# Optimization experiments

Hardware: AMD Instinct MI355X
Metric: run time of the kernel (lower is better)

The kernel has to match this reference:

```python
import jax, jax.numpy as jnp
import numpy as np

T, B, F, H = 128, 32768, 8, 64


def gru_step(h, x, Wih, Whh, bih, bhh):
    # PyTorch GRU cell, gate order (r, z, n)
    gi = x @ Wih.T + bih          # [B, 3H]
    gh = h @ Whh.T + bhh          # [B, 3H]
    i_r, i_z, i_n = jnp.split(gi, 3, axis=-1)
    h_r, h_z, h_n = jnp.split(gh, 3, axis=-1)
    r = jax.nn.sigmoid(i_r + h_r)
    z = jax.nn.sigmoid(i_z + h_z)
    n = jnp.tanh(i_n + r * h_n)
    return (1.0 - z) * n + z * h


def setup_inputs() -> dict:
    key = jax.random.key(0)
    ks = jax.random.split(key, 12)
    s = 0.1  # small init scale
    return {
        "inputs": jax.random.normal(ks[0], (T, B, F), jnp.float32),
        "target": jax.random.normal(ks[1], (T, B, F), jnp.float32),
        "enc_Wih": jax.random.normal(ks[2], (3 * H, F), jnp.float32) * s,
        "enc_Whh": jax.random.normal(ks[3], (3 * H, H), jnp.float32) * s,
        "enc_bih": jax.random.normal(ks[4], (3 * H,), jnp.float32) * s,
        "enc_bhh": jax.random.normal(ks[5], (3 * H,), jnp.float32) * s,
        "dec_Wih": jax.random.normal(ks[6], (3 * H, F), jnp.float32) * s,
        "dec_Whh": jax.random.normal(ks[7], (3 * H, H), jnp.float32) * s,
        "dec_bih": jax.random.normal(ks[8], (3 * H,), jnp.float32) * s,
        "dec_bhh": jax.random.normal(ks[9], (3 * H,), jnp.float32) * s,
        "out_W": jax.random.normal(ks[10], (F, H), jnp.float32) * s,
        "out_b": jax.random.normal(ks[11], (F,), jnp.float32) * s,
    }


def reference(inputs, target, enc_Wih, enc_Whh, enc_bih, enc_bhh,
              dec_Wih, dec_Whh, dec_bih, dec_bhh, out_W, out_b):
    batch = inputs.shape[1]
    # ---- Encoder: single-layer GRU over T steps, h0 = 0 ----
    h0 = jnp.zeros((batch, H), inputs.dtype)

    def enc_body(h, x_t):
        h = gru_step(h, x_t, enc_Wih, enc_Whh, enc_bih, enc_bhh)
        return h, None

    enc_hidden, _ = jax.lax.scan(enc_body, h0, inputs)

    # ---- Decoder: teacher forcing; input at t=0 is zeros, then target[t-1] ----
    dec_in = jnp.concatenate(
        [jnp.zeros((1, batch, target.shape[2]), target.dtype), target[:-1]], axis=0)

    def dec_body(h, x_t):
        h = gru_step(h, x_t, dec_Wih, dec_Whh, dec_bih, dec_bhh)
        y = h @ out_W.T + out_b  # [B, F]
        return h, y

    _, decoder_outputs = jax.lax.scan(dec_body, enc_hidden, dec_in)
    return decoder_outputs  # [T, B, F]
```

## Files before the change

### kernel.cpp

```cpp
#include <hip/hip_runtime.h>

#define T_STEPS 128
#define B_SIZE  32768
#define F_DIM   8
#define H_DIM   64

#define BLOCK_THREADS 128
#define GRID_BLOCKS   (B_SIZE / 16)

typedef float f32x4 __attribute__((ext_vector_type(4)));
typedef short bfrag __attribute__((ext_vector_type(8)));
typedef unsigned int u32x4 __attribute__((ext_vector_type(4)));

#define MFMA16(A, B, C) __builtin_amdgcn_mfma_f32_16x16x32_bf16((A), (B), (C), 0, 0, 0)

__device__ __forceinline__ short f2bf(float f) { return __builtin_bit_cast(short, (__bf16)f); }
__device__ __forceinline__ float4 ld4(const void* p) { return *(const float4*)p; }

constexpr float S1 = 1.4426950408889634f;
constexpr float S2 = 2.f * S1;


__global__ __launch_bounds__(BLOCK_THREADS, 3)
void seq2seq_split_kernel(const float* __restrict__ inputs, const float* __restrict__ target,
                          const float* __restrict__ eWih, const float* __restrict__ eWhh,
                          const float* __restrict__ ebih, const float* __restrict__ ebhh,
                          const float* __restrict__ dWih, const float* __restrict__ dWhh,
                          const float* __restrict__ dbih, const float* __restrict__ dbhh,
                          const float* __restrict__ oW, const float* __restrict__ ob,
                          float* __restrict__ out)
{
    __shared__ u32x4 sXT[2][6][64];
    __shared__ u32x4 sEx[2][2][64];

    const int tid  = threadIdx.x;
    const int lane = tid & 63;
    const int w    = tid >> 6;
    const int c    = lane & 15;
    const int g    = lane >> 4;
    const long samp = (long)blockIdx.x * 16 + c;

    bfrag wr[2][2], wz[2][2], whn[2][2];
    f32x4 bhn[2];

    auto load_phase = [&](const float* __restrict__ Wih, const float* __restrict__ Whh,
                          const float* __restrict__ bih, const float* __restrict__ bhh) {
        __syncthreads();
#pragma unroll
        for (int tl = 0; tl < 2; ++tl) {
            const int tt = 2 * w + tl;
            const int rowR = 16 * tt + c, rowZ = rowR + 64, rowN = rowR + 128;
#pragma unroll
            for (int j = 0; j < 2; ++j) {
                const int kt = (j == 0) ? w : 1 - w;
                bfrag fr, fz, fn;
#pragma unroll
                for (int e = 0; e < 8; ++e) {
                    const int k = 32 * kt + 16 * (e >> 2) + 4 * g + (e & 3);
                    fr[e] = f2bf(Whh[rowR * H_DIM + k] * S1);
                    fz[e] = f2bf(Whh[rowZ * H_DIM + k] * S1);
                    fn[e] = f2bf(Whh[rowN * H_DIM + k] * S2);
                }
                wr[tl][j] = fr; wz[tl][j] = fz; whn[tl][j] = fn;
            }
            bfrag xr, xz, xnw;
#pragma unroll
            for (int e = 0; e < 8; ++e) {
                const int k = 16 * (e >> 2) + 4 * g + (e & 3);
                float vr = 0.f, vz = 0.f, vn = 0.f;
                if (k < F_DIM) {
                    vr = Wih[rowR * F_DIM + k]; vz = Wih[rowZ * F_DIM + k]; vn = Wih[rowN * F_DIM + k];
                } else if (k == F_DIM) {
                    vr = bih[rowR] + bhh[rowR]; vz = bih[rowZ] + bhh[rowZ]; vn = bih[rowN];
                }
                xr[e] = f2bf(vr * S1); xz[e] = f2bf(vz * S1); xnw[e] = f2bf(vn * S2);
            }
            sXT[w][3 * tl + 0][lane] = __builtin_bit_cast(u32x4, xr);
            sXT[w][3 * tl + 1][lane] = __builtin_bit_cast(u32x4, xz);
            sXT[w][3 * tl + 2][lane] = __builtin_bit_cast(u32x4, xnw);
#pragma unroll
            for (int r4 = 0; r4 < 4; ++r4) bhn[tl][r4] = bhh[128 + 16 * tt + 4 * g + r4] * S2;
        }
        __syncthreads();
    };

    f32x4 hc[2] = {{0.f, 0.f, 0.f, 0.f}, {0.f, 0.f, 0.f, 0.f}};
    bfrag hl = (bfrag){0, 0, 0, 0, 0, 0, 0, 0};
    bfrag ho = (bfrag){0, 0, 0, 0, 0, 0, 0, 0};
    bfrag bx0 = (bfrag){0, 0, 0, 0, 0, 0, 0, 0};
    if (g == 2) bx0[0] = f2bf(1.f);

    const u32x4* xt = &sXT[w][0][lane];

    auto step = [&](const bfrag bx) {
#pragma unroll
        for (int tl = 0; tl < 2; ++tl) {
            const bfrag xr  = __builtin_bit_cast(bfrag, xt[(3 * tl + 0) * 64]);
            const bfrag xz  = __builtin_bit_cast(bfrag, xt[(3 * tl + 1) * 64]);
            const bfrag xnw = __builtin_bit_cast(bfrag, xt[(3 * tl + 2) * 64]);
            f32x4 aR = {0.f, 0.f, 0.f, 0.f}, aZ = {0.f, 0.f, 0.f, 0.f};
            f32x4 aIN = {0.f, 0.f, 0.f, 0.f};
            f32x4 aHN = bhn[tl];
            aR = MFMA16(wr[tl][0], hl, aR);  aR = MFMA16(wr[tl][1], ho, aR);  aR = MFMA16(xr, bx, aR);
            aZ = MFMA16(wz[tl][0], hl, aZ);  aZ = MFMA16(wz[tl][1], ho, aZ);  aZ = MFMA16(xz, bx, aZ);
            aHN = MFMA16(whn[tl][0], hl, aHN); aHN = MFMA16(whn[tl][1], ho, aHN);
            aIN = MFMA16(xnw, bx, aIN);
#pragma unroll
            for (int r4 = 0; r4 < 4; ++r4) {
                const float rg = __builtin_amdgcn_rcpf(1.f + __builtin_amdgcn_exp2f(-aR[r4]));
                const float zg = __builtin_amdgcn_rcpf(1.f + __builtin_amdgcn_exp2f(-aZ[r4]));
                const float np = aIN[r4] + rg * aHN[r4];
                const float ng = 1.f - 2.f * __builtin_amdgcn_rcpf(__builtin_amdgcn_exp2f(np) + 1.f);
                hc[tl][r4] = ng + zg * (hc[tl][r4] - ng);
            }
        }
        bfrag nl;
#pragma unroll
        for (int e = 0; e < 8; ++e) nl[e] = f2bf(hc[e >> 2][e & 3]);
        hl = nl;
    };

    load_phase(eWih, eWhh, ebih, ebhh);
    int p = 0;
    const unsigned istep = B_SIZE * F_DIM * 4;
    unsigned ioff = (unsigned)((samp * F_DIM + 4 * g) * 4);
    float4 xn = make_float4(0.f, 0.f, 0.f, 0.f);
    if (g < 2) xn = ld4((const char*)inputs + ioff);
    ioff += istep;
#pragma unroll 1
    for (int t = 0; t < T_STEPS; ++t) {
        const float4 xv = xn;
        if (g < 2 && t + 1 < T_STEPS) xn = ld4((const char*)inputs + ioff);
        ioff += istep;
        bfrag bx = bx0;
        if (g < 2) { bx[0] = f2bf(xv.x); bx[1] = f2bf(xv.y); bx[2] = f2bf(xv.z); bx[3] = f2bf(xv.w); }
        step(bx);
        sEx[p][w][lane] = __builtin_bit_cast(u32x4, hl);
        __syncthreads();
        ho = __builtin_bit_cast(bfrag, sEx[p][w ^ 1][lane]);
        p ^= 1;
    }

    load_phase(dWih, dWhh, dbih, dbhh);
    bfrag wo[2];
    f32x4 obv;
#pragma unroll
    for (int j = 0; j < 2; ++j)
#pragma unroll
        for (int e = 0; e < 8; ++e) {
            const int k = 32 * j + 16 * (e >> 2) + 4 * g + (e & 3);
            wo[j][e] = f2bf((c < F_DIM) ? oW[c * H_DIM + k] : 0.f);
        }
#pragma unroll
    for (int r4 = 0; r4 < 4; ++r4) obv[r4] = (g < 2) ? ob[4 * g + r4] : 0.f;

    unsigned toff = (unsigned)((samp * F_DIM + 4 * g) * 4);
    unsigned ooff = toff;
    xn = make_float4(0.f, 0.f, 0.f, 0.f);
#pragma unroll 1
    for (int t = 0; t < T_STEPS; ++t) {
        const float4 xv = xn;
        if (g < 2 && t + 1 < T_STEPS) xn = ld4((const char*)target + toff);
        toff += istep;
        bfrag bx = bx0;
        if (g < 2) { bx[0] = f2bf(xv.x); bx[1] = f2bf(xv.y); bx[2] = f2bf(xv.z); bx[3] = f2bf(xv.w); }
        step(bx);
        sEx[p][w][lane] = __builtin_bit_cast(u32x4, hl);
        __syncthreads();
        ho = __builtin_bit_cast(bfrag, sEx[p][w ^ 1][lane]);
        p ^= 1;
        if (w == 0) {
            f32x4 aO = obv;
            aO = MFMA16(wo[0], hl, aO);
            aO = MFMA16(wo[1], ho, aO);
            if (g < 2) {
                float4 o; o.x = aO[0]; o.y = aO[1]; o.z = aO[2]; o.w = aO[3];
                *(float4*)((char*)out + ooff) = o;
            }
        }
        ooff += istep;
    }
}

extern "C" void kernel_launch(void* const* d_in, const int* in_sizes, int n_in,
                              void* d_out, int out_size, void* d_ws, size_t ws_size,
                              hipStream_t stream) {
    (void)in_sizes; (void)n_in; (void)d_ws; (void)ws_size; (void)out_size;
    const float* inputs = (const float*)d_in[0];
    const float* target = (const float*)d_in[1];
    const float* eWih   = (const float*)d_in[2];
    const float* eWhh   = (const float*)d_in[3];
    const float* ebih   = (const float*)d_in[4];
    const float* ebhh   = (const float*)d_in[5];
    const float* dWih   = (const float*)d_in[6];
    const float* dWhh   = (const float*)d_in[7];
    const float* dbih   = (const float*)d_in[8];
    const float* dbhh   = (const float*)d_in[9];
    const float* oW     = (const float*)d_in[10];
    const float* ob     = (const float*)d_in[11];
    float* out = (float*)d_out;

    seq2seq_split_kernel<<<dim3(GRID_BLOCKS), dim3(BLOCK_THREADS), 0, stream>>>(
        inputs, target, eWih, eWhh, ebih, ebhh, dWih, dWhh, dbih, dbhh, oW, ob, out);
}
```

Measured before the change: 479.3 us.

## Process two 16-sample groups per block for instruction-level parallelism

Each block now handles 32 samples as two independent 16-sample groups, interleaving their GRU steps so MFMA and transcendental chains from one group can overlap with the other. This also amortizes the per-step barrier across twice the work and halves the grid. The input-weight fragments are kept in registers instead of being reread from LDS each step. In exchange register pressure rises and launch bounds drop to 2 blocks per SIMD, which lowers occupancy.

Measured after the change: 506.5 us. 1.06x slower.

```diff
diff --git a/kernel.cpp b/kernel.cpp
--- a/kernel.cpp
+++ b/kernel.cpp
@@ -6,7 +6,7 @@
 #define H_DIM   64
 
 #define BLOCK_THREADS 128
-#define GRID_BLOCKS   (B_SIZE / 16)
+#define GRID_BLOCKS   (B_SIZE / 32)
 
 typedef float f32x4 __attribute__((ext_vector_type(4)));
 typedef short bfrag __attribute__((ext_vector_type(8)));
@@ -21,31 +21,29 @@
 constexpr float S2 = 2.f * S1;
 
 
-__global__ __launch_bounds__(BLOCK_THREADS, 3)
-void seq2seq_split_kernel(const float* __restrict__ inputs, const float* __restrict__ target,
-                          const float* __restrict__ eWih, const float* __restrict__ eWhh,
-                          const float* __restrict__ ebih, const float* __restrict__ ebhh,
-                          const float* __restrict__ dWih, const float* __restrict__ dWhh,
-                          const float* __restrict__ dbih, const float* __restrict__ dbhh,
-                          const float* __restrict__ oW, const float* __restrict__ ob,
-                          float* __restrict__ out)
+__global__ __launch_bounds__(BLOCK_THREADS, 2)
+void seq2seq_ilp2_kernel(const float* __restrict__ inputs, const float* __restrict__ target,
+                         const float* __restrict__ eWih, const float* __restrict__ eWhh,
+                         const float* __restrict__ ebih, const float* __restrict__ ebhh,
+                         const float* __restrict__ dWih, const float* __restrict__ dWhh,
+                         const float* __restrict__ dbih, const float* __restrict__ dbhh,
+                         const float* __restrict__ oW, const float* __restrict__ ob,
+                         float* __restrict__ out)
 {
-    __shared__ u32x4 sXT[2][6][64];
-    __shared__ u32x4 sEx[2][2][64];
+    __shared__ u32x4 sEx[2][2][2][64];
 
     const int tid  = threadIdx.x;
     const int lane = tid & 63;
     const int w    = tid >> 6;
     const int c    = lane & 15;
     const int g    = lane >> 4;
-    const long samp = (long)blockIdx.x * 16 + c;
 
     bfrag wr[2][2], wz[2][2], whn[2][2];
+    bfrag xr[2], xz[2], xnw[2];
     f32x4 bhn[2];
 
     auto load_phase = [&](const float* __restrict__ Wih, const float* __restrict__ Whh,
                           const float* __restrict__ bih, const float* __restrict__ bhh) {
-        __syncthreads();
 #pragma unroll
         for (int tl = 0; tl < 2; ++tl) {
             const int tt = 2 * w + tl;
@@ -63,7 +61,7 @@
                 }
                 wr[tl][j] = fr; wz[tl][j] = fz; whn[tl][j] = fn;
             }
-            bfrag xr, xz, xnw;
+            bfrag axr, axz, axn;
 #pragma unroll
             for (int e = 0; e < 8; ++e) {
                 const int k = 16 * (e >> 2) + 4 * g + (e & 3);
@@ -73,71 +71,74 @@
                 } else if (k == F_DIM) {
                     vr = bih[rowR] + bhh[rowR]; vz = bih[rowZ] + bhh[rowZ]; vn = bih[rowN];
                 }
-                xr[e] = f2bf(vr * S1); xz[e] = f2bf(vz * S1); xnw[e] = f2bf(vn * S2);
-            }
-            sXT[w][3 * tl + 0][lane] = __builtin_bit_cast(u32x4, xr);
-            sXT[w][3 * tl + 1][lane] = __builtin_bit_cast(u32x4, xz);
-            sXT[w][3 * tl + 2][lane] = __builtin_bit_cast(u32x4, xnw);
+                axr[e] = f2bf(vr * S1); axz[e] = f2bf(vz * S1); axn[e] = f2bf(vn * S2);
+            }
+            xr[tl] = axr; xz[tl] = axz; xnw[tl] = axn;
 #pragma unroll
             for (int r4 = 0; r4 < 4; ++r4) bhn[tl][r4] = bhh[128 + 16 * tt + 4 * g + r4] * S2;
         }
-        __syncthreads();
     };
 
-    f32x4 hc[2] = {{0.f, 0.f, 0.f, 0.f}, {0.f, 0.f, 0.f, 0.f}};
-    bfrag hl = (bfrag){0, 0, 0, 0, 0, 0, 0, 0};
-    bfrag ho = (bfrag){0, 0, 0, 0, 0, 0, 0, 0};
-    bfrag bx0 = (bfrag){0, 0, 0, 0, 0, 0, 0, 0};
+    f32x4 hc[2][2] = {{{0.f,0.f,0.f,0.f},{0.f,0.f,0.f,0.f}},
+                      {{0.f,0.f,0.f,0.f},{0.f,0.f,0.f,0.f}}};
+    bfrag hl[2] = {(bfrag){0,0,0,0,0,0,0,0}, (bfrag){0,0,0,0,0,0,0,0}};
+    bfrag ho[2] = {(bfrag){0,0,0,0,0,0,0,0}, (bfrag){0,0,0,0,0,0,0,0}};
+    bfrag bx0 = (bfrag){0,0,0,0,0,0,0,0};
     if (g == 2) bx0[0] = f2bf(1.f);
 
-    const u32x4* xt = &sXT[w][0][lane];
-
-    auto step = [&](const bfrag bx) {
+    auto step = [&](bfrag& HL, const bfrag HO, const bfrag bx, f32x4 (&HC)[2]) {
 #pragma unroll
         for (int tl = 0; tl < 2; ++tl) {
-            const bfrag xr  = __builtin_bit_cast(bfrag, xt[(3 * tl + 0) * 64]);
-            const bfrag xz  = __builtin_bit_cast(bfrag, xt[(3 * tl + 1) * 64]);
-            const bfrag xnw = __builtin_bit_cast(bfrag, xt[(3 * tl + 2) * 64]);
-            f32x4 aR = {0.f, 0.f, 0.f, 0.f}, aZ = {0.f, 0.f, 0.f, 0.f};
-            f32x4 aIN = {0.f, 0.f, 0.f, 0.f};
+            f32x4 aR = {0.f,0.f,0.f,0.f}, aZ = {0.f,0.f,0.f,0.f};
+            f32x4 aIN = {0.f,0.f,0.f,0.f};
             f32x4 aHN = bhn[tl];
-            aR = MFMA16(wr[tl][0], hl, aR);  aR = MFMA16(wr[tl][1], ho, aR);  aR = MFMA16(xr, bx, aR);
-            aZ = MFMA16(wz[tl][0], hl, aZ);  aZ = MFMA16(wz[tl][1], ho, aZ);  aZ = MFMA16(xz, bx, aZ);
-            aHN = MFMA16(whn[tl][0], hl, aHN); aHN = MFMA16(whn[tl][1], ho, aHN);
-            aIN = MFMA16(xnw, bx, aIN);
+            aR = MFMA16(wr[tl][0], HL, aR);   aR = MFMA16(wr[tl][1], HO, aR);   aR = MFMA16(xr[tl], bx, aR);
+            aZ = MFMA16(wz[tl][0], HL, aZ);   aZ = MFMA16(wz[tl][1], HO, aZ);   aZ = MFMA16(xz[tl], bx, aZ);
+            aHN = MFMA16(whn[tl][0], HL, aHN); aHN = MFMA16(whn[tl][1], HO, aHN);
+            aIN = MFMA16(xnw[tl], bx, aIN);
 #pragma unroll
             for (int r4 = 0; r4 < 4; ++r4) {
                 const float rg = __builtin_amdgcn_rcpf(1.f + __builtin_amdgcn_exp2f(-aR[r4]));
                 const float zg = __builtin_amdgcn_rcpf(1.f + __builtin_amdgcn_exp2f(-aZ[r4]));
                 const float np = aIN[r4] + rg * aHN[r4];
                 const float ng = 1.f - 2.f * __builtin_amdgcn_rcpf(__builtin_amdgcn_exp2f(np) + 1.f);
-                hc[tl][r4] = ng + zg * (hc[tl][r4] - ng);
+                HC[tl][r4] = ng + zg * (HC[tl][r4] - ng);
             }
         }
         bfrag nl;
 #pragma unroll
-        for (int e = 0; e < 8; ++e) nl[e] = f2bf(hc[e >> 2][e & 3]);
-        hl = nl;
+        for (int e = 0; e < 8; ++e) nl[e] = f2bf(HC[e >> 2][e & 3]);
+        HL = nl;
     };
+
+    auto make_bx = [&](const float4 xv) {
+        bfrag bx = bx0;
+        if (g < 2) { bx[0] = f2bf(xv.x); bx[1] = f2bf(xv.y); bx[2] = f2bf(xv.z); bx[3] = f2bf(xv.w); }
+        return bx;
+    };
+
+    const unsigned istep = B_SIZE * F_DIM * 4;
+    const unsigned off0  = ((unsigned)(blockIdx.x * 32 + c) * F_DIM + 4 * g) * 4;
 
     load_phase(eWih, eWhh, ebih, ebhh);
     int p = 0;
-    const unsigned istep = B_SIZE * F_DIM * 4;
-    unsigned ioff = (unsigned)((samp * F_DIM + 4 * g) * 4);
-    float4 xn = make_float4(0.f, 0.f, 0.f, 0.f);
-    if (g < 2) xn = ld4((const char*)inputs + ioff);
-    ioff += istep;
+    float4 xn[2] = {make_float4(0.f,0.f,0.f,0.f), make_float4(0.f,0.f,0.f,0.f)};
+    if (g < 2) { xn[0] = ld4((const char*)inputs + off0); xn[1] = ld4((const char*)inputs + off0 + 512); }
+    unsigned ioff = off0 + istep;
 #pragma unroll 1
     for (int t = 0; t < T_STEPS; ++t) {
-        const float4 xv = xn;
-        if (g < 2 && t + 1 < T_STEPS) xn = ld4((const char*)inputs + ioff);
+#pragma unroll
+        for (int grp = 0; grp < 2; ++grp) {
+            const float4 xv = xn[grp];
+            if (g < 2 && t + 1 < T_STEPS) xn[grp] = ld4((const char*)inputs + ioff + 512 * grp);
+            step(hl[grp], ho[grp], make_bx(xv), hc[grp]);
+        }
         ioff += istep;
-        bfrag bx = bx0;
-        if (g < 2) { bx[0] = f2bf(xv.x); bx[1] = f2bf(xv.y); bx[2] = f2bf(xv.z); bx[3] = f2bf(xv.w); }
-        step(bx);
-        sEx[p][w][lane] = __builtin_bit_cast(u32x4, hl);
+        sEx[p][w][0][lane] = __builtin_bit_cast(u32x4, hl[0]);
+        sEx[p][w][1][lane] = __builtin_bit_cast(u32x4, hl[1]);
         __syncthreads();
-        ho = __builtin_bit_cast(bfrag, sEx[p][w ^ 1][lane]);
+        ho[0] = __builtin_bit_cast(bfrag, sEx[p][w ^ 1][0][lane]);
+        ho[1] = __builtin_bit_cast(bfrag, sEx[p][w ^ 1][1][lane]);
         p ^= 1;
     }
 
@@ -154,28 +155,34 @@
 #pragma unroll
     for (int r4 = 0; r4 < 4; ++r4) obv[r4] = (g < 2) ? ob[4 * g + r4] : 0.f;
 
-    unsigned toff = (unsigned)((samp * F_DIM + 4 * g) * 4);
-    unsigned ooff = toff;
-    xn = make_float4(0.f, 0.f, 0.f, 0.f);
+    unsigned toff = off0;
+    unsigned ooff = off0;
+    xn[0] = xn[1] = make_float4(0.f, 0.f, 0.f, 0.f);
 #pragma unroll 1
     for (int t = 0; t < T_STEPS; ++t) {
-        const float4 xv = xn;
-        if (g < 2 && t + 1 < T_STEPS) xn = ld4((const char*)target + toff);
+#pragma unroll
+        for (int grp = 0; grp < 2; ++grp) {
+            const float4 xv = xn[grp];
+            if (g < 2 && t + 1 < T_STEPS) xn[grp] = ld4((const char*)target + toff + 512 * grp);
+            step(hl[grp], ho[grp], make_bx(xv), hc[grp]);
+        }
         toff += istep;
-        bfrag bx = bx0;
-        if (g < 2) { bx[0] = f2bf(xv.x); bx[1] = f2bf(xv.y); bx[2] = f2bf(xv.z); bx[3] = f2bf(xv.w); }
-        step(bx);
-        sEx[p][w][lane] = __builtin_bit_cast(u32x4, hl);
+        sEx[p][w][0][lane] = __builtin_bit_cast(u32x4, hl[0]);
+        sEx[p][w][1][lane] = __builtin_bit_cast(u32x4, hl[1]);
         __syncthreads();
-        ho = __builtin_bit_cast(bfrag, sEx[p][w ^ 1][lane]);
+        ho[0] = __builtin_bit_cast(bfrag, sEx[p][w ^ 1][0][lane]);
+        ho[1] = __builtin_bit_cast(bfrag, sEx[p][w ^ 1][1][lane]);
         p ^= 1;
         if (w == 0) {
-            f32x4 aO = obv;
-            aO = MFMA16(wo[0], hl, aO);
-            aO = MFMA16(wo[1], ho, aO);
-            if (g < 2) {
-                float4 o; o.x = aO[0]; o.y = aO[1]; o.z = aO[2]; o.w = aO[3];
-                *(float4*)((char*)out + ooff) = o;
+#pragma unroll
+            for (int grp = 0; grp < 2; ++grp) {
+                f32x4 aO = obv;
+                aO = MFMA16(wo[0], hl[grp], aO);
+                aO = MFMA16(wo[1], ho[grp], aO);
+                if (g < 2) {
+                    float4 o; o.x = aO[0]; o.y = aO[1]; o.z = aO[2]; o.w = aO[3];
+                    *(float4*)((char*)out + ooff + 512 * grp) = o;
+                }
             }
         }
         ooff += istep;
@@ -200,6 +207,6 @@
     const float* ob     = (const float*)d_in[11];
     float* out = (float*)d_out;
 
-    seq2seq_split_kernel<<<dim3(GRID_BLOCKS), dim3(BLOCK_THREADS), 0, stream>>>(
+    seq2seq_ilp2_kernel<<<dim3(GRID_BLOCKS), dim3(BLOCK_THREADS), 0, stream>>>(
         inputs, target, eWih, eWhh, ebih, ebhh, dWih, dWhh, dbih, dbhh, oW, ob, out);
 }
```

## Keep input-weight fragments in registers, use raw LDS barrier, alternate output wave

Applied to the files above, without the earlier changes.

Moves the input-projection weight fragments out of shared memory into registers, which removes six LDS reads per step. It replaces __syncthreads in the recurrent loops with an inline s_waitcnt lgkmcnt(0) plus s_barrier, so the barrier does not also wait on outstanding global loads. The decoder output projection now alternates between the two waves each step, so wave 0 no longer carries it every step. Launch bounds rise from 3 to 4 blocks per CU, which adds register pressure and a risk of spills.

Result: slower. 657.0 us (+37.1%).

```diff
diff --git a/kernel.cpp b/kernel.cpp
--- a/kernel.cpp
+++ b/kernel.cpp
@@ -14,6 +14,8 @@
 
 #define MFMA16(A, B, C) __builtin_amdgcn_mfma_f32_16x16x32_bf16((A), (B), (C), 0, 0, 0)
 
+#define LDS_BARRIER() asm volatile("s_waitcnt lgkmcnt(0)\n\ts_barrier" ::: "memory")
+
 __device__ __forceinline__ short f2bf(float f) { return __builtin_bit_cast(short, (__bf16)f); }
 __device__ __forceinline__ float4 ld4(const void* p) { return *(const float4*)p; }
 
@@ -21,16 +23,15 @@
 constexpr float S2 = 2.f * S1;
 
 
-__global__ __launch_bounds__(BLOCK_THREADS, 3)
-void seq2seq_split_kernel(const float* __restrict__ inputs, const float* __restrict__ target,
-                          const float* __restrict__ eWih, const float* __restrict__ eWhh,
-                          const float* __restrict__ ebih, const float* __restrict__ ebhh,
-                          const float* __restrict__ dWih, const float* __restrict__ dWhh,
-                          const float* __restrict__ dbih, const float* __restrict__ dbhh,
-                          const float* __restrict__ oW, const float* __restrict__ ob,
-                          float* __restrict__ out)
+__global__ __launch_bounds__(BLOCK_THREADS, 4)
+void seq2seq_rawbar_kernel(const float* __restrict__ inputs, const float* __restrict__ target,
+                           const float* __restrict__ eWih, const float* __restrict__ eWhh,
+                           const float* __restrict__ ebih, const float* __restrict__ ebhh,
+                           const float* __restrict__ dWih, const float* __restrict__ dWhh,
+                           const float* __restrict__ dbih, const float* __restrict__ dbhh,
+                           const float* __restrict__ oW, const float* __restrict__ ob,
+                           float* __restrict__ out)
 {
-    __shared__ u32x4 sXT[2][6][64];
     __shared__ u32x4 sEx[2][2][64];
 
     const int tid  = threadIdx.x;
@@ -38,14 +39,13 @@
     const int w    = tid >> 6;
     const int c    = lane & 15;
     const int g    = lane >> 4;
-    const long samp = (long)blockIdx.x * 16 + c;
 
     bfrag wr[2][2], wz[2][2], whn[2][2];
+    bfrag xr[2], xz[2], xnw[2];
     f32x4 bhn[2];
 
     auto load_phase = [&](const float* __restrict__ Wih, const float* __restrict__ Whh,
                           const float* __restrict__ bih, const float* __restrict__ bhh) {
-        __syncthreads();
 #pragma unroll
         for (int tl = 0; tl < 2; ++tl) {
             const int tt = 2 * w + tl;
@@ -63,7 +63,7 @@
                 }
                 wr[tl][j] = fr; wz[tl][j] = fz; whn[tl][j] = fn;
             }
-            bfrag xr, xz, xnw;
+            bfrag axr, axz, axn;
 #pragma unroll
             for (int e = 0; e < 8; ++e) {
                 const int k = 16 * (e >> 2) + 4 * g + (e & 3);
@@ -73,38 +73,30 @@
                 } else if (k == F_DIM) {
                     vr = bih[rowR] + bhh[rowR]; vz = bih[rowZ] + bhh[rowZ]; vn = bih[rowN];
                 }
-                xr[e] = f2bf(vr * S1); xz[e] = f2bf(vz * S1); xnw[e] = f2bf(vn * S2);
-            }
-            sXT[w][3 * tl + 0][lane] = __builtin_bit_cast(u32x4, xr);
-            sXT[w][3 * tl + 1][lane] = __builtin_bit_cast(u32x4, xz);
-            sXT[w][3 * tl + 2][lane] = __builtin_bit_cast(u32x4, xnw);
+                axr[e] = f2bf(vr * S1); axz[e] = f2bf(vz * S1); axn[e] = f2bf(vn * S2);
+            }
+            xr[tl] = axr; xz[tl] = axz; xnw[tl] = axn;
 #pragma unroll
             for (int r4 = 0; r4 < 4; ++r4) bhn[tl][r4] = bhh[128 + 16 * tt + 4 * g + r4] * S2;
         }
-        __syncthreads();
     };
 
-    f32x4 hc[2] = {{0.f, 0.f, 0.f, 0.f}, {0.f, 0.f, 0.f, 0.f}};
-    bfrag hl = (bfrag){0, 0, 0, 0, 0, 0, 0, 0};
-    bfrag ho = (bfrag){0, 0, 0, 0, 0, 0, 0, 0};
-    bfrag bx0 = (bfrag){0, 0, 0, 0, 0, 0, 0, 0};
+    f32x4 hc[2] = {{0.f,0.f,0.f,0.f},{0.f,0.f,0.f,0.f}};
+    bfrag hl = (bfrag){0,0,0,0,0,0,0,0};
+    bfrag ho = (bfrag){0,0,0,0,0,0,0,0};
+    bfrag bx0 = (bfrag){0,0,0,0,0,0,0,0};
     if (g == 2) bx0[0] = f2bf(1.f);
 
-    const u32x4* xt = &sXT[w][0][lane];
-
     auto step = [&](const bfrag bx) {
 #pragma unroll
         for (int tl = 0; tl < 2; ++tl) {
-            const bfrag xr  = __builtin_bit_cast(bfrag, xt[(3 * tl + 0) * 64]);
-            const bfrag xz  = __builtin_bit_cast(bfrag, xt[(3 * tl + 1) * 64]);
-            const bfrag xnw = __builtin_bit_cast(bfrag, xt[(3 * tl + 2) * 64]);
-            f32x4 aR = {0.f, 0.f, 0.f, 0.f}, aZ = {0.f, 0.f, 0.f, 0.f};
-            f32x4 aIN = {0.f, 0.f, 0.f, 0.f};
+            f32x4 aR = {0.f,0.f,0.f,0.f}, aZ = {0.f,0.f,0.f,0.f};
+            f32x4 aIN = {0.f,0.f,0.f,0.f};
             f32x4 aHN = bhn[tl];
-            aR = MFMA16(wr[tl][0], hl, aR);  aR = MFMA16(wr[tl][1], ho, aR);  aR = MFMA16(xr, bx, aR);
-            aZ = MFMA16(wz[tl][0], hl, aZ);  aZ = MFMA16(wz[tl][1], ho, aZ);  aZ = MFMA16(xz, bx, aZ);
+            aR = MFMA16(wr[tl][0], hl, aR);   aR = MFMA16(wr[tl][1], ho, aR);   aR = MFMA16(xr[tl], bx, aR);
+            aZ = MFMA16(wz[tl][0], hl, aZ);   aZ = MFMA16(wz[tl][1], ho, aZ);   aZ = MFMA16(xz[tl], bx, aZ);
             aHN = MFMA16(whn[tl][0], hl, aHN); aHN = MFMA16(whn[tl][1], ho, aHN);
-            aIN = MFMA16(xnw, bx, aIN);
+            aIN = MFMA16(xnw[tl], bx, aIN);
 #pragma unroll
             for (int r4 = 0; r4 < 4; ++r4) {
                 const float rg = __builtin_amdgcn_rcpf(1.f + __builtin_amdgcn_exp2f(-aR[r4]));
@@ -120,59 +112,68 @@
         hl = nl;
     };
 
+    auto make_bx = [&](const float4 xv) {
+        bfrag bx = bx0;
+        if (g < 2) { bx[0] = f2bf(xv.x); bx[1] = f2bf(xv.y); bx[2] = f2bf(xv.z); bx[3] = f2bf(xv.w); }
+        return bx;
+    };
+
+    const unsigned istep = B_SIZE * F_DIM * 4;
+    const unsigned off0  = ((unsigned)(blockIdx.x * 16 + c) * F_DIM + 4 * g) * 4;
+
     load_phase(eWih, eWhh, ebih, ebhh);
+    __syncthreads();
     int p = 0;
-    const unsigned istep = B_SIZE * F_DIM * 4;
-    unsigned ioff = (unsigned)((samp * F_DIM + 4 * g) * 4);
     float4 xn = make_float4(0.f, 0.f, 0.f, 0.f);
-    if (g < 2) xn = ld4((const char*)inputs + ioff);
-    ioff += istep;
+    if (g < 2) xn = ld4((const char*)inputs + off0);
+    unsigned ioff = off0 + istep;
 #pragma unroll 1
     for (int t = 0; t < T_STEPS; ++t) {
         const float4 xv = xn;
         if (g < 2 && t + 1 < T_STEPS) xn = ld4((const char*)inputs + ioff);
         ioff += istep;
-        bfrag bx = bx0;
-        if (g < 2) { bx[0] = f2bf(xv.x); bx[1] = f2bf(xv.y); bx[2] = f2bf(xv.z); bx[3] = f2bf(xv.w); }
-        step(bx);
+        step(make_bx(xv));
         sEx[p][w][lane] = __builtin_bit_cast(u32x4, hl);
-        __syncthreads();
+        LDS_BARRIER();
         ho = __builtin_bit_cast(bfrag, sEx[p][w ^ 1][lane]);
         p ^= 1;
     }
 
+    __syncthreads();
     load_phase(dWih, dWhh, dbih, dbhh);
-    bfrag wo[2];
+    bfrag wo_own, wo_oth;
     f32x4 obv;
 #pragma unroll
-    for (int j = 0; j < 2; ++j)
+    for (int j = 0; j < 2; ++j) {
+        bfrag f;
 #pragma unroll
         for (int e = 0; e < 8; ++e) {
-            const int k = 32 * j + 16 * (e >> 2) + 4 * g + (e & 3);
-            wo[j][e] = f2bf((c < F_DIM) ? oW[c * H_DIM + k] : 0.f);
-        }
+            const int k = 32 * ((j == 0) ? w : 1 - w) + 16 * (e >> 2) + 4 * g + (e & 3);
+            f[e] = f2bf((c < F_DIM) ? oW[c * H_DIM + k] : 0.f);
+        }
+        if (j == 0) wo_own = f; else wo_oth = f;
+    }
 #pragma unroll
     for (int r4 = 0; r4 < 4; ++r4) obv[r4] = (g < 2) ? ob[4 * g + r4] : 0.f;
-
-    unsigned toff = (unsigned)((samp * F_DIM + 4 * g) * 4);
-    unsigned ooff = toff;
+    __syncthreads();
+
+    unsigned toff = off0;
+    unsigned ooff = off0;
     xn = make_float4(0.f, 0.f, 0.f, 0.f);
 #pragma unroll 1
     for (int t = 0; t < T_STEPS; ++t) {
         const float4 xv = xn;
         if (g < 2 && t + 1 < T_STEPS) xn = ld4((const char*)target + toff);
         toff += istep;
-        bfrag bx = bx0;
-        if (g < 2) { bx[0] = f2bf(xv.x); bx[1] = f2bf(xv.y); bx[2] = f2bf(xv.z); bx[3] = f2bf(xv.w); }
-        step(bx);
+        step(make_bx(xv));
         sEx[p][w][lane] = __builtin_bit_cast(u32x4, hl);
-        __syncthreads();
+        LDS_BARRIER();
         ho = __builtin_bit_cast(bfrag, sEx[p][w ^ 1][lane]);
         p ^= 1;
-        if (w == 0) {
+        if (((t + w) & 1) == 0) {
             f32x4 aO = obv;
-            aO = MFMA16(wo[0], hl, aO);
-            aO = MFMA16(wo[1], ho, aO);
+            aO = MFMA16(wo_own, hl, aO);
+            aO = MFMA16(wo_oth, ho, aO);
             if (g < 2) {
                 float4 o; o.x = aO[0]; o.y = aO[1]; o.z = aO[2]; o.w = aO[3];
                 *(float4*)((char*)out + ooff) = o;
@@ -200,6 +201,6 @@
     const float* ob     = (const float*)d_in[11];
     float* out = (float*)d_out;
 
-    seq2seq_split_kernel<<<dim3(GRID_BLOCKS), dim3(BLOCK_THREADS), 0, stream>>>(
+    seq2seq_rawbar_kernel<<<dim3(GRID_BLOCKS), dim3(BLOCK_THREADS), 0, stream>>>(
         inputs, target, eWih, eWhh, ebih, ebhh, dWih, dWhh, dbih, dbhh, oW, ob, out);
 }
```
